# Performance work log

Measured on AMD Instinct MI355X. Metric: run time of the kernel, lower is better.

The kernel has to match this reference:

```python
import jax, jax.numpy as jnp
import numpy as np

D_MODEL = 1024
N_HEADS = 16
D_FF = 4096
EPS = 1e-5


def setup_inputs() -> dict:
    key = jax.random.key(0)
    ks = jax.random.split(key, 10)
    B, S, D, F = 4, 2048, D_MODEL, D_FF
    s = 0.02
    return {
        "x": jax.random.normal(ks[0], (B, S, D), jnp.float32),
        "Wq": jax.random.normal(ks[1], (D, D), jnp.float32) * s,
        "bq": jnp.zeros((D,), jnp.float32),
        "Wk": jax.random.normal(ks[2], (D, D), jnp.float32) * s,
        "bk": jnp.zeros((D,), jnp.float32),
        "Wv": jax.random.normal(ks[3], (D, D), jnp.float32) * s,
        "bv": jnp.zeros((D,), jnp.float32),
        "Wo": jax.random.normal(ks[4], (D, D), jnp.float32) * s,
        "bo": jnp.zeros((D,), jnp.float32),
        "ln1_g": jnp.ones((D,), jnp.float32),
        "ln1_b": jnp.zeros((D,), jnp.float32),
        "ln2_g": jnp.ones((D,), jnp.float32),
        "ln2_b": jnp.zeros((D,), jnp.float32),
        "W1": jax.random.normal(ks[5], (D, F), jnp.float32) * s,
        "b1": jnp.zeros((F,), jnp.float32),
        "W2": jax.random.normal(ks[6], (F, D), jnp.float32) * s,
        "b2": jnp.zeros((D,), jnp.float32),
    }


def _layernorm(x, g, b):
    mu = jnp.mean(x, axis=-1, keepdims=True)
    var = jnp.mean(jnp.square(x - mu), axis=-1, keepdims=True)
    return (x - mu) * jax.lax.rsqrt(var + EPS) * g + b


def _attention(x, Wq, bq, Wk, bk, Wv, bv, Wo, bo):
    B, S, D = x.shape
    H, dk = N_HEADS, D // N_HEADS
    q = (x @ Wq + bq).reshape(B, S, H, dk).transpose(0, 2, 1, 3)  # bhsd
    k = (x @ Wk + bk).reshape(B, S, H, dk).transpose(0, 2, 1, 3)
    v = (x @ Wv + bv).reshape(B, S, H, dk).transpose(0, 2, 1, 3)
    scale = 1.0 / np.sqrt(dk)
    scores = jnp.einsum("bhqd,bhkd->bhqk", q, k) * scale
    causal = jnp.tril(jnp.ones((S, S), bool))
    scores = jnp.where(causal, scores, -jnp.inf)
    attn = jax.nn.softmax(scores, axis=-1)
    out = jnp.einsum("bhqk,bhkd->bhqd", attn, v)
    out = out.transpose(0, 2, 1, 3).reshape(B, S, D)
    return out @ Wo + bo


def reference(x, Wq, bq, Wk, bk, Wv, bv, Wo, bo, ln1_g, ln1_b, ln2_g, ln2_b, W1, b1, W2, b2):
    # Pre-LN: x -> LN -> attn -> +x -> LN -> FFN -> +x  (dropout = eval/identity)
    attn_out = _attention(_layernorm(x, ln1_g, ln1_b), Wq, bq, Wk, bk, Wv, bv, Wo, bo)
    x = x + attn_out
    h = _layernorm(x, ln2_g, ln2_b)
    ffn = jax.nn.gelu(h @ W1 + b1, approximate=False) @ W2 + b2
    return x + ffn
```

## Files before the change

kernel.cpp:

```cpp
#include <hip/hip_runtime.h>
#include <hip/hip_bf16.h>
#include <math.h>

typedef __attribute__((ext_vector_type(8))) short short8;
typedef __attribute__((ext_vector_type(4))) float floatx4;
typedef __attribute__((ext_vector_type(4))) short short4v;

#define D_MODEL 1024
#define N_HEADS 16
#define DK 64
#define D_FF 4096
#define BB 4
#define SS 2048
#define NTOK (BB * SS)
#define LN_EPS 1e-5f
#define SCL 0.18033688011112042f

static __device__ __forceinline__ short f2bf(float f) {
  union { float f; unsigned int u; } v;
  v.f = f;
  unsigned int u = v.u;
  unsigned int r = u + 0x7fffu + ((u >> 16) & 1u);
  return (short)(r >> 16);
}

#define GLL16(g, l)                                                            \
  __builtin_amdgcn_global_load_lds(                                            \
      (const __attribute__((address_space(1))) void*)(g),                      \
      (__attribute__((address_space(3))) void*)(l), 16, 0, 0)

__global__ __launch_bounds__(256) void ln_kernel(const float* __restrict__ x,
                                                 const float* __restrict__ g,
                                                 const float* __restrict__ b,
                                                 short* __restrict__ out) {
  int row = blockIdx.x;
  int t = threadIdx.x;
  const float4* rp = (const float4*)(x + (size_t)row * D_MODEL);
  float4 v = rp[t];
  float s = v.x + v.y + v.z + v.w;
  float ss = v.x * v.x + v.y * v.y + v.z * v.z + v.w * v.w;
#pragma unroll
  for (int off = 32; off >= 1; off >>= 1) {
    s += __shfl_xor(s, off, 64);
    ss += __shfl_xor(ss, off, 64);
  }
  __shared__ float red[8];
  int wv = t >> 6;
  if ((t & 63) == 0) { red[wv] = s; red[wv + 4] = ss; }
  __syncthreads();
  s = red[0] + red[1] + red[2] + red[3];
  ss = red[4] + red[5] + red[6] + red[7];
  float mu = s * (1.0f / D_MODEL);
  float var = ss * (1.0f / D_MODEL) - mu * mu;
  float rstd = rsqrtf(var + LN_EPS);
  float4 gv = ((const float4*)g)[t];
  float4 bv = ((const float4*)b)[t];
  short4v o;
  o.x = f2bf((v.x - mu) * rstd * gv.x + bv.x);
  o.y = f2bf((v.y - mu) * rstd * gv.y + bv.y);
  o.z = f2bf((v.z - mu) * rstd * gv.z + bv.z);
  o.w = f2bf((v.w - mu) * rstd * gv.w + bv.w);
  *(short4v*)(out + (size_t)row * D_MODEL + t * 4) = o;
}

__global__ __launch_bounds__(256) void wconvert_all(
    const float* __restrict__ Wq, const float* __restrict__ Wk,
    const float* __restrict__ Wv, const float* __restrict__ Wo,
    const float* __restrict__ W1, const float* __restrict__ W2,
    const float* __restrict__ bq, const float* __restrict__ bk,
    const float* __restrict__ bv,
    short* __restrict__ wqkv_t, short* __restrict__ wo_t,
    short* __restrict__ w1_t, short* __restrict__ w2_t,
    float* __restrict__ bqkv) {
  __shared__ float tile[64][65];
  int id = blockIdx.x;
  int t = threadIdx.x;
  if (id == 3072) {
    for (int i = t; i < 1024; i += 256) {
      bqkv[i] = bq[i];
      bqkv[1024 + i] = bk[i];
      bqkv[2048 + i] = bv[i];
    }
    return;
  }
  const float* W;
  short* Wt;
  int K, N, tid;
  if (id < 1024) {
    int wsel = id >> 8;
    tid = id & 255;
    K = 1024; N = 1024;
    W = wsel == 0 ? Wq : wsel == 1 ? Wk : wsel == 2 ? Wv : Wo;
    Wt = wsel < 3 ? wqkv_t + (size_t)wsel * 1024 * 1024 : wo_t;
  } else if (id < 2048) {
    tid = id - 1024; K = 1024; N = 4096; W = W1; Wt = w1_t;
  } else {
    tid = id - 2048; K = 4096; N = 1024; W = W2; Wt = w2_t;
  }
  int ntn = N >> 6;
  int n0 = (tid % ntn) * 64, k0 = (tid / ntn) * 64;
  int c = t & 63, r0 = t >> 6;
#pragma unroll
  for (int i = 0; i < 16; i++) {
    int r = r0 + i * 4;
    tile[r][c] = W[(size_t)(k0 + r) * N + n0 + c];
  }
  __syncthreads();
#pragma unroll
  for (int i = 0; i < 16; i++) {
    int r = r0 + i * 4;
    Wt[(size_t)(n0 + r) * K + k0 + c] = f2bf(tile[c][r]);
  }
}

template <int MODE>
__global__ __launch_bounds__(256, 4) void gemm_bt(const short* __restrict__ A,
                                                  const short* __restrict__ Bt,
                                                  const float* __restrict__ bias,
                                                  const float* __restrict__ res,
                                                  float* __restrict__ outf,
                                                  short* __restrict__ outb,
                                                  int M, int N, int K) {
  __shared__ short As[128 * 64];
  __shared__ short Bs[128 * 64];
  int t = threadIdx.x;
  int w = t >> 6, l = t & 63;
  int lm = l & 15, lq = l >> 4;
  int m0 = blockIdx.y * 128, n0 = blockIdx.x * 128;
  floatx4 acc[4][4] = {};
  int l3 = l >> 3;
  int c7 = ((l & 7) ^ l3) * 8;
  const short* aA = A + (size_t)(m0 + w * 8 + l3) * K + c7;
  const short* aB = Bt + (size_t)(n0 + w * 8 + l3) * K + c7;
  int wm = (w & 1) * 64, wn = (w >> 1) * 64;
  int sw = lm & 7;

  for (int kt = 0; kt < K; kt += 64) {
#pragma unroll
    for (int j = 0; j < 4; j++) {
      GLL16(aA + (size_t)(j * 32) * K, As + (j * 32 + w * 8) * 64);
      GLL16(aB + (size_t)(j * 32) * K, Bs + (j * 32 + w * 8) * 64);
    }
    aA += 64;
    aB += 64;
    __syncthreads();
#pragma unroll
    for (int kk = 0; kk < 2; kk++) {
      int rdoff = ((kk * 4 + lq) ^ sw) * 8;
      short8 af[4], bfr[4];
#pragma unroll
      for (int mi = 0; mi < 4; mi++)
        af[mi] = *(const short8*)&As[(wm + mi * 16 + lm) * 64 + rdoff];
#pragma unroll
      for (int ni = 0; ni < 4; ni++)
        bfr[ni] = *(const short8*)&Bs[(wn + ni * 16 + lm) * 64 + rdoff];
#pragma unroll
      for (int mi = 0; mi < 4; mi++)
#pragma unroll
        for (int ni = 0; ni < 4; ni++)
          acc[mi][ni] = __builtin_amdgcn_mfma_f32_16x16x32_bf16(af[mi], bfr[ni],
                                                                acc[mi][ni], 0, 0, 0);
    }
    __syncthreads();
  }

#pragma unroll
  for (int mi = 0; mi < 4; mi++) {
#pragma unroll
    for (int ni = 0; ni < 4; ni++) {
      int col = n0 + wn + ni * 16 + lm;
      float bcol = bias[col];
#pragma unroll
      for (int r = 0; r < 4; r++) {
        int row = m0 + wm + mi * 16 + lq * 4 + r;
        float v = acc[mi][ni][r] + bcol;
        size_t idx = (size_t)row * N + col;
        if (MODE == 0) {
          outb[idx] = f2bf(v);
        } else if (MODE == 1) {
          outf[idx] = v + res[idx];
        } else {
          float vc = v + 0.044715f * v * v * v;
          float e = __builtin_amdgcn_exp2f(2.302265246314f * vc);
          float ge = v * e * __builtin_amdgcn_rcpf(e + 1.0f);
          outb[idx] = f2bf(ge);
        }
      }
    }
  }
}

__global__ __launch_bounds__(256) void vtrans(const short* __restrict__ qkv,
                                              short* __restrict__ vt) {
  __shared__ short Ls[64][72];
  int t = threadIdx.x;
  int s0 = blockIdx.x * 64;
  int bh = blockIdx.y;
  int b = bh >> 4, h = bh & 15;
  const short* vsrc = qkv + (size_t)b * SS * 3072 + 2048 + h * 64;
#pragma unroll
  for (int it = 0; it < 2; it++) {
    int idx = it * 256 + t;
    int sr = idx >> 3, ch = idx & 7;
    *(short8*)&Ls[sr][ch * 8] =
        *(const short8*)&vsrc[(size_t)(s0 + sr) * 3072 + ch * 8];
  }
  __syncthreads();
  int d = t >> 2, sb = (t & 3) * 16;
  short tmp[16];
#pragma unroll
  for (int j = 0; j < 16; j++) tmp[j] = Ls[sb + j][d];
  short8* dst = (short8*)&vt[(size_t)bh * DK * SS + (size_t)d * SS + s0 + sb];
  dst[0] = *(short8*)&tmp[0];
  dst[1] = *(short8*)&tmp[8];
}

__global__ __launch_bounds__(256) void attn_kernel(const short* __restrict__ qkv,
                                                   const short* __restrict__ vt,
                                                   short* __restrict__ o) {
  __shared__ short Qs[128 * 64];
  __shared__ short Ks[64 * 64];
  __shared__ short Vs[64 * 64];
  __shared__ short Ps[128 * 72];
  int t = threadIdx.x, w = t >> 6, l = t & 63;
  int bh = blockIdx.x;
  int p = blockIdx.y;
  int b = bh >> 4, h = bh & 15;
  const short* qbase = qkv + (size_t)b * SS * 3072 + h * DK;
  const short* kbase = qbase + 1024;
  const short* vbase = vt + (size_t)bh * DK * SS;
  short* obase = o + (size_t)b * SS * D_MODEL + h * DK;
  int l7 = l & 7, l3 = l >> 3;
  int c7 = (l7 ^ l3) * 8;
  int lm = l & 15, lq = l >> 4;
  int swq = lm & 7;

  for (int ph = 0; ph < 2; ph++) {
    int qi = ph ? (15 - p) : p;
    int q0 = qi * 128;
#pragma unroll
    for (int j = 0; j < 4; j++) {
      int r8 = w * 32 + j * 8;
      GLL16(qbase + (size_t)(q0 + r8 + l3) * 3072 + c7, Qs + r8 * 64);
    }
    __syncthreads();
    short8 aq[2][2];
#pragma unroll
    for (int m = 0; m < 2; m++)
#pragma unroll
      for (int hf = 0; hf < 2; hf++)
        aq[m][hf] = *(const short8*)&Qs[(w * 32 + m * 16 + lm) * 64 +
                                        ((hf * 4 + lq) ^ swq) * 8];

    floatx4 accO[2][4] = {};
    float lst[2][4] = {};
    int wrow_min = q0 + w * 32;
    int wrow_max = wrow_min + 31;
    int ntile = 2 * qi + 2;
    for (int kt = 0; kt < ntile; kt++) {
      int k0 = kt * 64;
      __syncthreads();
#pragma unroll
      for (int j = 0; j < 2; j++) {
        int r8 = (w * 2 + j) * 8;
        GLL16(kbase + (size_t)(k0 + r8 + l3) * 3072 + c7, Ks + r8 * 64);
        GLL16(vbase + (size_t)(r8 + l3) * SS + k0 + c7, Vs + r8 * 64);
      }
      __syncthreads();

      if (k0 <= wrow_max) {
        floatx4 sc[2][4];
#pragma unroll
        for (int nb = 0; nb < 4; nb++) {
          short8 k0f = *(const short8*)&Ks[(nb * 16 + lm) * 64 + (lq ^ swq) * 8];
          short8 k1f =
              *(const short8*)&Ks[(nb * 16 + lm) * 64 + ((4 + lq) ^ swq) * 8];
#pragma unroll
          for (int m = 0; m < 2; m++) {
            floatx4 z = {};
            z = __builtin_amdgcn_mfma_f32_16x16x32_bf16(aq[m][0], k0f, z, 0, 0, 0);
            z = __builtin_amdgcn_mfma_f32_16x16x32_bf16(aq[m][1], k1f, z, 0, 0, 0);
            sc[m][nb] = z;
          }
        }
        if (k0 + 63 <= wrow_min) {
#pragma unroll
          for (int m = 0; m < 2; m++)
#pragma unroll
            for (int r = 0; r < 4; r++)
#pragma unroll
              for (int nb = 0; nb < 4; nb++) {
                float pv = exp2f(sc[m][nb][r] * SCL);
                sc[m][nb][r] = pv;
                lst[m][r] += pv;
              }
        } else {
#pragma unroll
          for (int m = 0; m < 2; m++)
#pragma unroll
            for (int r = 0; r < 4; r++) {
              int rowg = q0 + w * 32 + m * 16 + lq * 4 + r;
#pragma unroll
              for (int nb = 0; nb < 4; nb++) {
                int colg = k0 + nb * 16 + lm;
                float pv = (colg > rowg) ? 0.f : exp2f(sc[m][nb][r] * SCL);
                sc[m][nb][r] = pv;
                lst[m][r] += pv;
              }
            }
        }
#pragma unroll
        for (int m = 0; m < 2; m++)
#pragma unroll
          for (int nb = 0; nb < 4; nb++)
#pragma unroll
            for (int r = 0; r < 4; r++) {
              union { float f; unsigned int u; } cv;
              cv.f = sc[m][nb][r];
              Ps[(w * 32 + m * 16 + lq * 4 + r) * 72 + nb * 16 + lm] =
                  (short)(cv.u >> 16);
            }
        short8 pa[2][2];
#pragma unroll
        for (int m = 0; m < 2; m++)
#pragma unroll
          for (int hf = 0; hf < 2; hf++)
            pa[m][hf] =
                *(const short8*)&Ps[(w * 32 + m * 16 + lm) * 72 + hf * 32 + lq * 8];
#pragma unroll
        for (int nb = 0; nb < 4; nb++) {
          short8 v0f = *(const short8*)&Vs[(nb * 16 + lm) * 64 + (lq ^ swq) * 8];
          short8 v1f =
              *(const short8*)&Vs[(nb * 16 + lm) * 64 + ((4 + lq) ^ swq) * 8];
#pragma unroll
          for (int m = 0; m < 2; m++) {
            accO[m][nb] = __builtin_amdgcn_mfma_f32_16x16x32_bf16(pa[m][0], v0f,
                                                                  accO[m][nb], 0, 0, 0);
            accO[m][nb] = __builtin_amdgcn_mfma_f32_16x16x32_bf16(pa[m][1], v1f,
                                                                  accO[m][nb], 0, 0, 0);
          }
        }
      }
    }
#pragma unroll
    for (int m = 0; m < 2; m++)
#pragma unroll
      for (int r = 0; r < 4; r++) {
        float s = lst[m][r];
        s += __shfl_xor(s, 1, 64);
        s += __shfl_xor(s, 2, 64);
        s += __shfl_xor(s, 4, 64);
        s += __shfl_xor(s, 8, 64);
        float inv = 1.0f / s;
        int rowg = q0 + w * 32 + m * 16 + lq * 4 + r;
#pragma unroll
        for (int nb = 0; nb < 4; nb++)
          obase[(size_t)rowg * D_MODEL + nb * 16 + lm] = f2bf(accO[m][nb][r] * inv);
      }
  }
}

extern "C" void kernel_launch(void* const* d_in, const int* in_sizes, int n_in,
                              void* d_out, int out_size, void* d_ws, size_t ws_size,
                              hipStream_t stream) {
  const float* x = (const float*)d_in[0];
  const float* Wq = (const float*)d_in[1];
  const float* bq = (const float*)d_in[2];
  const float* Wk = (const float*)d_in[3];
  const float* bk = (const float*)d_in[4];
  const float* Wv = (const float*)d_in[5];
  const float* bv = (const float*)d_in[6];
  const float* Wo = (const float*)d_in[7];
  const float* bo = (const float*)d_in[8];
  const float* ln1g = (const float*)d_in[9];
  const float* ln1b = (const float*)d_in[10];
  const float* ln2g = (const float*)d_in[11];
  const float* ln2b = (const float*)d_in[12];
  const float* W1 = (const float*)d_in[13];
  const float* b1 = (const float*)d_in[14];
  const float* W2 = (const float*)d_in[15];
  const float* b2 = (const float*)d_in[16];
  float* out = (float*)d_out;

  short* wqkv_t = (short*)d_ws;
  short* wo_t = wqkv_t + 3072 * 1024;
  short* w1_t = wo_t + 1024 * 1024;
  short* w2_t = w1_t + 4096 * 1024;
  float* bqkv = (float*)(w2_t + 1024 * 4096);
  short* h_bf = (short*)(bqkv + 3072);
  short* qkvb = h_bf + (size_t)NTOK * D_MODEL;
  short* vtg = qkvb + (size_t)NTOK * 3072;
  short* ffn1 = qkvb;

  wconvert_all<<<3073, 256, 0, stream>>>(Wq, Wk, Wv, Wo, W1, W2, bq, bk, bv,
                                         wqkv_t, wo_t, w1_t, w2_t, bqkv);

  ln_kernel<<<NTOK, 256, 0, stream>>>(x, ln1g, ln1b, h_bf);

  gemm_bt<0><<<dim3(24, 64), 256, 0, stream>>>(h_bf, wqkv_t, bqkv, nullptr, nullptr,
                                               qkvb, NTOK, 3072, 1024);

  vtrans<<<dim3(SS / 64, 64), 256, 0, stream>>>(qkvb, vtg);

  attn_kernel<<<dim3(64, 8), 256, 0, stream>>>(qkvb, vtg, h_bf);

  gemm_bt<1><<<dim3(8, 64), 256, 0, stream>>>(h_bf, wo_t, bo, x, out, nullptr,
                                              NTOK, 1024, 1024);

  ln_kernel<<<NTOK, 256, 0, stream>>>(out, ln2g, ln2b, h_bf);

  gemm_bt<2><<<dim3(32, 64), 256, 0, stream>>>(h_bf, w1_t, b1, nullptr, nullptr,
                                               ffn1, NTOK, 4096, 1024);

  gemm_bt<1><<<dim3(8, 64), 256, 0, stream>>>(ffn1, w2_t, b2, out, out, nullptr,
                                              NTOK, 1024, 4096);
}
```

Before: 478.9 us.

## Transpose score MFMA, pack P writes, one q-tile per block with more blocks

The attention kernel swaps the MFMA operand order so each lane holds scores for a single query row across 4 keys. That lets P be written to shared memory as packed 64-bit stores, and the row-sum becomes one scalar per m-block reduced with two shuffles. The paired-tile loop that balanced causal work inside a block is removed: each block now handles one 128-row query tile, the grid doubles to 1024 blocks with heaviest tiles first, and launch bounds request 3 blocks per CU. The cost is that load balance now depends on the hardware scheduler instead of the explicit pairing, and the epilogue needs an extra shuffle to redistribute the inverse sums.

```diff
diff --git a/kernel.cpp b/kernel.cpp
--- a/kernel.cpp
+++ b/kernel.cpp
@@ -5,6 +5,7 @@
 typedef __attribute__((ext_vector_type(8))) short short8;
 typedef __attribute__((ext_vector_type(4))) float floatx4;
 typedef __attribute__((ext_vector_type(4))) short short4v;
+typedef __attribute__((ext_vector_type(2))) unsigned int uint2v;
 
 #define D_MODEL 1024
 #define N_HEADS 16
@@ -215,16 +216,16 @@
   dst[1] = *(short8*)&tmp[8];
 }
 
-__global__ __launch_bounds__(256) void attn_kernel(const short* __restrict__ qkv,
-                                                   const short* __restrict__ vt,
-                                                   short* __restrict__ o) {
+__global__ __launch_bounds__(256, 3) void attn_kernel(const short* __restrict__ qkv,
+                                                      const short* __restrict__ vt,
+                                                      short* __restrict__ o) {
   __shared__ short Qs[128 * 64];
   __shared__ short Ks[64 * 64];
   __shared__ short Vs[64 * 64];
   __shared__ short Ps[128 * 72];
   int t = threadIdx.x, w = t >> 6, l = t & 63;
   int bh = blockIdx.x;
-  int p = blockIdx.y;
+  int qi = 15 - blockIdx.y;
   int b = bh >> 4, h = bh & 15;
   const short* qbase = qkv + (size_t)b * SS * 3072 + h * DK;
   const short* kbase = qbase + 1024;
@@ -234,129 +235,127 @@
   int c7 = (l7 ^ l3) * 8;
   int lm = l & 15, lq = l >> 4;
   int swq = lm & 7;
-
-  for (int ph = 0; ph < 2; ph++) {
-    int qi = ph ? (15 - p) : p;
-    int q0 = qi * 128;
-#pragma unroll
-    for (int j = 0; j < 4; j++) {
-      int r8 = w * 32 + j * 8;
-      GLL16(qbase + (size_t)(q0 + r8 + l3) * 3072 + c7, Qs + r8 * 64);
-    }
+  int q0 = qi * 128;
+
+#pragma unroll
+  for (int j = 0; j < 4; j++) {
+    int r8 = w * 32 + j * 8;
+    GLL16(qbase + (size_t)(q0 + r8 + l3) * 3072 + c7, Qs + r8 * 64);
+  }
+  __syncthreads();
+  short8 aq[2][2];
+#pragma unroll
+  for (int m = 0; m < 2; m++)
+#pragma unroll
+    for (int hf = 0; hf < 2; hf++)
+      aq[m][hf] = *(const short8*)&Qs[(w * 32 + m * 16 + lm) * 64 +
+                                      ((hf * 4 + lq) ^ swq) * 8];
+
+  floatx4 accO[2][4] = {};
+  float lst[2] = {0.f, 0.f};
+  int qrow[2] = {q0 + w * 32 + lm, q0 + w * 32 + 16 + lm};
+  int wrow_min = q0 + w * 32;
+  int wrow_max = wrow_min + 31;
+  int ntile = 2 * qi + 2;
+  for (int kt = 0; kt < ntile; kt++) {
+    int k0 = kt * 64;
     __syncthreads();
-    short8 aq[2][2];
-#pragma unroll
-    for (int m = 0; m < 2; m++)
-#pragma unroll
-      for (int hf = 0; hf < 2; hf++)
-        aq[m][hf] = *(const short8*)&Qs[(w * 32 + m * 16 + lm) * 64 +
-                                        ((hf * 4 + lq) ^ swq) * 8];
-
-    floatx4 accO[2][4] = {};
-    float lst[2][4] = {};
-    int wrow_min = q0 + w * 32;
-    int wrow_max = wrow_min + 31;
-    int ntile = 2 * qi + 2;
-    for (int kt = 0; kt < ntile; kt++) {
-      int k0 = kt * 64;
-      __syncthreads();
-#pragma unroll
-      for (int j = 0; j < 2; j++) {
-        int r8 = (w * 2 + j) * 8;
-        GLL16(kbase + (size_t)(k0 + r8 + l3) * 3072 + c7, Ks + r8 * 64);
-        GLL16(vbase + (size_t)(r8 + l3) * SS + k0 + c7, Vs + r8 * 64);
+#pragma unroll
+    for (int j = 0; j < 2; j++) {
+      int r8 = (w * 2 + j) * 8;
+      GLL16(kbase + (size_t)(k0 + r8 + l3) * 3072 + c7, Ks + r8 * 64);
+      GLL16(vbase + (size_t)(r8 + l3) * SS + k0 + c7, Vs + r8 * 64);
+    }
+    __syncthreads();
+
+    if (k0 <= wrow_max) {
+      floatx4 sc[4][2];
+#pragma unroll
+      for (int sb = 0; sb < 4; sb++) {
+        short8 k0f = *(const short8*)&Ks[(sb * 16 + lm) * 64 + (lq ^ swq) * 8];
+        short8 k1f =
+            *(const short8*)&Ks[(sb * 16 + lm) * 64 + ((4 + lq) ^ swq) * 8];
+#pragma unroll
+        for (int m = 0; m < 2; m++) {
+          floatx4 z = {};
+          z = __builtin_amdgcn_mfma_f32_16x16x32_bf16(k0f, aq[m][0], z, 0, 0, 0);
+          z = __builtin_amdgcn_mfma_f32_16x16x32_bf16(k1f, aq[m][1], z, 0, 0, 0);
+          sc[sb][m] = z;
+        }
       }
-      __syncthreads();
-
-      if (k0 <= wrow_max) {
-        floatx4 sc[2][4];
-#pragma unroll
-        for (int nb = 0; nb < 4; nb++) {
-          short8 k0f = *(const short8*)&Ks[(nb * 16 + lm) * 64 + (lq ^ swq) * 8];
-          short8 k1f =
-              *(const short8*)&Ks[(nb * 16 + lm) * 64 + ((4 + lq) ^ swq) * 8];
-#pragma unroll
-          for (int m = 0; m < 2; m++) {
-            floatx4 z = {};
-            z = __builtin_amdgcn_mfma_f32_16x16x32_bf16(aq[m][0], k0f, z, 0, 0, 0);
-            z = __builtin_amdgcn_mfma_f32_16x16x32_bf16(aq[m][1], k1f, z, 0, 0, 0);
-            sc[m][nb] = z;
-          }
-        }
-        if (k0 + 63 <= wrow_min) {
+      if (k0 + 63 <= wrow_min) {
+#pragma unroll
+        for (int sb = 0; sb < 4; sb++)
 #pragma unroll
           for (int m = 0; m < 2; m++)
 #pragma unroll
-            for (int r = 0; r < 4; r++)
-#pragma unroll
-              for (int nb = 0; nb < 4; nb++) {
-                float pv = exp2f(sc[m][nb][r] * SCL);
-                sc[m][nb][r] = pv;
-                lst[m][r] += pv;
-              }
-        } else {
+            for (int r = 0; r < 4; r++) {
+              float pv = exp2f(sc[sb][m][r] * SCL);
+              sc[sb][m][r] = pv;
+              lst[m] += pv;
+            }
+      } else {
+#pragma unroll
+        for (int sb = 0; sb < 4; sb++) {
+          int sbase = k0 + sb * 16 + lq * 4;
 #pragma unroll
           for (int m = 0; m < 2; m++)
 #pragma unroll
             for (int r = 0; r < 4; r++) {
-              int rowg = q0 + w * 32 + m * 16 + lq * 4 + r;
-#pragma unroll
-              for (int nb = 0; nb < 4; nb++) {
-                int colg = k0 + nb * 16 + lm;
-                float pv = (colg > rowg) ? 0.f : exp2f(sc[m][nb][r] * SCL);
-                sc[m][nb][r] = pv;
-                lst[m][r] += pv;
-              }
+              float pv = (sbase + r > qrow[m]) ? 0.f : exp2f(sc[sb][m][r] * SCL);
+              sc[sb][m][r] = pv;
+              lst[m] += pv;
             }
         }
-#pragma unroll
-        for (int m = 0; m < 2; m++)
-#pragma unroll
-          for (int nb = 0; nb < 4; nb++)
-#pragma unroll
-            for (int r = 0; r < 4; r++) {
-              union { float f; unsigned int u; } cv;
-              cv.f = sc[m][nb][r];
-              Ps[(w * 32 + m * 16 + lq * 4 + r) * 72 + nb * 16 + lm] =
-                  (short)(cv.u >> 16);
-            }
-        short8 pa[2][2];
-#pragma unroll
-        for (int m = 0; m < 2; m++)
-#pragma unroll
-          for (int hf = 0; hf < 2; hf++)
-            pa[m][hf] =
-                *(const short8*)&Ps[(w * 32 + m * 16 + lm) * 72 + hf * 32 + lq * 8];
-#pragma unroll
-        for (int nb = 0; nb < 4; nb++) {
-          short8 v0f = *(const short8*)&Vs[(nb * 16 + lm) * 64 + (lq ^ swq) * 8];
-          short8 v1f =
-              *(const short8*)&Vs[(nb * 16 + lm) * 64 + ((4 + lq) ^ swq) * 8];
-#pragma unroll
-          for (int m = 0; m < 2; m++) {
-            accO[m][nb] = __builtin_amdgcn_mfma_f32_16x16x32_bf16(pa[m][0], v0f,
-                                                                  accO[m][nb], 0, 0, 0);
-            accO[m][nb] = __builtin_amdgcn_mfma_f32_16x16x32_bf16(pa[m][1], v1f,
-                                                                  accO[m][nb], 0, 0, 0);
-          }
+      }
+#pragma unroll
+      for (int m = 0; m < 2; m++)
+#pragma unroll
+        for (int sb = 0; sb < 4; sb++) {
+          union { float f; unsigned int u; } c0, c1, c2, c3;
+          c0.f = sc[sb][m][0]; c1.f = sc[sb][m][1];
+          c2.f = sc[sb][m][2]; c3.f = sc[sb][m][3];
+          uint2v pk;
+          pk.x = (c0.u >> 16) | (c1.u & 0xFFFF0000u);
+          pk.y = (c2.u >> 16) | (c3.u & 0xFFFF0000u);
+          *(uint2v*)&Ps[(w * 32 + m * 16 + lm) * 72 + sb * 16 + lq * 4] = pk;
+        }
+      short8 pa[2][2];
+#pragma unroll
+      for (int m = 0; m < 2; m++)
+#pragma unroll
+        for (int hf = 0; hf < 2; hf++)
+          pa[m][hf] =
+              *(const short8*)&Ps[(w * 32 + m * 16 + lm) * 72 + hf * 32 + lq * 8];
+#pragma unroll
+      for (int nb = 0; nb < 4; nb++) {
+        short8 v0f = *(const short8*)&Vs[(nb * 16 + lm) * 64 + (lq ^ swq) * 8];
+        short8 v1f =
+            *(const short8*)&Vs[(nb * 16 + lm) * 64 + ((4 + lq) ^ swq) * 8];
+#pragma unroll
+        for (int m = 0; m < 2; m++) {
+          accO[m][nb] = __builtin_amdgcn_mfma_f32_16x16x32_bf16(pa[m][0], v0f,
+                                                                accO[m][nb], 0, 0, 0);
+          accO[m][nb] = __builtin_amdgcn_mfma_f32_16x16x32_bf16(pa[m][1], v1f,
+                                                                accO[m][nb], 0, 0, 0);
         }
       }
     }
-#pragma unroll
-    for (int m = 0; m < 2; m++)
-#pragma unroll
-      for (int r = 0; r < 4; r++) {
-        float s = lst[m][r];
-        s += __shfl_xor(s, 1, 64);
-        s += __shfl_xor(s, 2, 64);
-        s += __shfl_xor(s, 4, 64);
-        s += __shfl_xor(s, 8, 64);
-        float inv = 1.0f / s;
-        int rowg = q0 + w * 32 + m * 16 + lq * 4 + r;
-#pragma unroll
-        for (int nb = 0; nb < 4; nb++)
-          obase[(size_t)rowg * D_MODEL + nb * 16 + lm] = f2bf(accO[m][nb][r] * inv);
-      }
+  }
+#pragma unroll
+  for (int m = 0; m < 2; m++) {
+    float s = lst[m];
+    s += __shfl_xor(s, 16, 64);
+    s += __shfl_xor(s, 32, 64);
+    float inv = 1.0f / s;
+#pragma unroll
+    for (int r = 0; r < 4; r++) {
+      float invr = __shfl(inv, (l & 48) | (lq * 4 + r), 64);
+      int rowg = q0 + w * 32 + m * 16 + lq * 4 + r;
+#pragma unroll
+      for (int nb = 0; nb < 4; nb++)
+        obase[(size_t)rowg * D_MODEL + nb * 16 + lm] = f2bf(accO[m][nb][r] * invr);
+    }
   }
 }
 
@@ -402,7 +401,7 @@
 
   vtrans<<<dim3(SS / 64, 64), 256, 0, stream>>>(qkvb, vtg);
 
-  attn_kernel<<<dim3(64, 8), 256, 0, stream>>>(qkvb, vtg, h_bf);
+  attn_kernel<<<dim3(64, 16), 256, 0, stream>>>(qkvb, vtg, h_bf);
 
   gemm_bt<1><<<dim3(8, 64), 256, 0, stream>>>(h_bf, wo_t, bo, x, out, nullptr,
                                               NTOK, 1024, 1024);
```

Result: no change. 479.7 us (+0.2%).
